# Optimization experiments

Measured on AMD Instinct MI355X. Metric: run time of the kernel, lower is better.

The kernel has to match this reference:

```python
import jax, jax.numpy as jnp
import numpy as np

B, S, D_MODEL = 2, 2048, 2048
N_HEADS, N_KV_HEADS = 32, 8
HEAD_DIM = D_MODEL // N_HEADS  # 64


def setup_inputs() -> dict:
    key = jax.random.key(0)
    ks = jax.random.split(key, 7)
    # rope frequencies (as in standard RoPE; values just need to be the right shape)
    inv_freq = 1.0 / (10000.0 ** (jnp.arange(0, HEAD_DIM, 2, dtype=jnp.float32) / HEAD_DIM))
    t = jnp.arange(S, dtype=jnp.float32)
    freqs = t[:, None] * inv_freq[None, :]  # (S, head_dim//2)
    scale = 0.02
    return {
        "x": jax.random.normal(ks[0], (B, S, D_MODEL), jnp.float32),
        "cos": jnp.cos(freqs),
        "sin": jnp.sin(freqs),
        "Wq": jax.random.normal(ks[1], (N_HEADS * HEAD_DIM, D_MODEL), jnp.float32) * scale,
        "Wk": jax.random.normal(ks[2], (N_KV_HEADS * HEAD_DIM, D_MODEL), jnp.float32) * scale,
        "Wv": jax.random.normal(ks[3], (N_KV_HEADS * HEAD_DIM, D_MODEL), jnp.float32) * scale,
        "Wo": jax.random.normal(ks[4], (D_MODEL, D_MODEL), jnp.float32) * scale,
    }


def _apply_rope(x, cos, sin):
    # x: (B, H, S, D); cos/sin: (S, D//2)
    d = x.shape[-1]
    x1, x2 = x[..., : d // 2], x[..., d // 2:]
    c = cos[None, None]
    s = sin[None, None]
    return jnp.concatenate([x1 * c - x2 * s, x1 * s + x2 * c], axis=-1)


def reference(x, cos, sin, Wq, Wk, Wv, Wo):
    b, s, _ = x.shape
    hd = 2 * cos.shape[-1]
    h = Wq.shape[0] // hd
    kv = Wk.shape[0] // hd
    g = h // kv  # query heads per kv head

    q = (x @ Wq.T).reshape(b, s, h, hd).transpose(0, 2, 1, 3)    # (b,h,s,d)
    k = (x @ Wk.T).reshape(b, s, kv, hd).transpose(0, 2, 1, 3)   # (b,kv,s,d)
    v = (x @ Wv.T).reshape(b, s, kv, hd).transpose(0, 2, 1, 3)

    q = _apply_rope(q, cos, sin)
    k = _apply_rope(k, cos, sin)

    # GQA: group query heads instead of materializing repeated K/V
    qg = q.reshape(b, kv, g, s, hd)
    scale = 1.0 / jnp.sqrt(jnp.asarray(hd, x.dtype))
    scores = jnp.einsum('bkgsd,bktd->bkgst', qg, k) * scale      # (b,kv,g,s,s)
    causal = jnp.arange(s)[:, None] >= jnp.arange(s)[None, :]
    scores = jnp.where(causal[None, None, None], scores, jnp.asarray(-jnp.inf, scores.dtype))
    attn = jax.nn.softmax(scores, axis=-1)
    out = jnp.einsum('bkgst,bktd->bkgsd', attn, v)               # (b,kv,g,s,d)
    out = out.reshape(b, h, s, hd).transpose(0, 2, 1, 3).reshape(b, s, h * hd)
    return out @ Wo.T
```

## Files before the change

kernel.cpp:

```cpp
#include <hip/hip_runtime.h>
#include <hip/hip_bf16.h>

typedef __bf16 bf16;
typedef __attribute__((ext_vector_type(8))) __bf16 bf16x8;
typedef __attribute__((ext_vector_type(4))) __bf16 bf16x4;
typedef __attribute__((ext_vector_type(4))) float f32x4;

#define B_SZ 2
#define S_SZ 2048
#define D_SZ 2048
#define H_SZ 32
#define KV_SZ 8
#define HD_SZ 64
#define M_SZ (B_SZ * S_SZ)
#define NQKV 3072

#define GLDS(g, s) __builtin_amdgcn_global_load_lds( \
    (const __attribute__((address_space(1))) void*)(g), \
    (__attribute__((address_space(3))) void*)(s), 16, 0, 0)

__device__ __forceinline__ void bar_lgkm() {
    asm volatile("s_waitcnt lgkmcnt(0)\n\ts_barrier" ::: "memory");
}

__global__ void cvt_all(const float* __restrict__ x, const float* __restrict__ Wq,
                        const float* __restrict__ Wk, const float* __restrict__ Wv,
                        const float* __restrict__ Wo,
                        bf16* __restrict__ xb, bf16* __restrict__ Wf, bf16* __restrict__ wob,
                        int nx, int n1, int n2) {
    int i = blockIdx.x * blockDim.x + threadIdx.x;
    const float* src; bf16* dst; int off;
    if (i < nx)                 { src = x;  dst = xb; off = i; }
    else {
        int j = i - nx;
        if (j < n1)             { src = Wq; dst = Wf; off = j; }
        else if (j < n1 + n2)   { src = Wk; dst = Wf + (size_t)4 * n1; off = j - n1; }
        else if (j < n1 + 2*n2) { src = Wv; dst = Wf + (size_t)4 * (n1 + n2); off = j - n1 - n2; }
        else if (j < 2*n1+2*n2) { src = Wo; dst = wob; off = j - n1 - 2 * n2; }
        else return;
    }
    float4 v = ((const float4*)src)[off];
    bf16x4 o;
    o.x = (bf16)v.x; o.y = (bf16)v.y; o.z = (bf16)v.z; o.w = (bf16)v.w;
    ((bf16x4*)dst)[off] = o;
}

#define GEMM_CORE2(A_, B_, Kdim)                                                 \
    const int tid  = threadIdx.x;                                                \
    const int w    = tid >> 6;                                                   \
    const int lane = tid & 63;                                                   \
    const int c = lane & 15, quad = lane >> 4;                                   \
    const int g8 = lane >> 3;                                                    \
    const int chs = ((lane & 7) ^ g8) * 8;                                       \
    const int rowBase = blockIdx.y * 128;                                        \
    const int colBase = blockIdx.x * 128;                                        \
    const bf16* Ag = A_ + (size_t)(rowBase + w * 64 + g8) * Kdim + chs;          \
    const bf16* Bg = B_ + (size_t)(colBase + w * 64 + g8) * Kdim + chs;          \
    bf16* sAw = As + (w * 64) * 64;                                              \
    bf16* sBw = Bs + (w * 64) * 64;                                              \
    f32x4 acc[4][8] = {};                                                        \
    for (int k0 = 0; k0 < Kdim; k0 += 64) {                                      \
        _Pragma("unroll")                                                        \
        for (int j = 0; j < 8; j++) {                                            \
            GLDS(Ag + (size_t)(j * 8) * Kdim + k0, sAw + j * 512);               \
            GLDS(Bg + (size_t)(j * 8) * Kdim + k0, sBw + j * 512);               \
        }                                                                        \
        __syncthreads();                                                         \
        _Pragma("unroll")                                                        \
        for (int ks = 0; ks < 2; ks++) {                                         \
            bf16x8 af[4], bfr[8];                                                \
            _Pragma("unroll")                                                    \
            for (int mi = 0; mi < 4; mi++)                                       \
                af[mi] = *(const bf16x8*)(As + (w * 64 + mi * 16 + c) * 64       \
                                          + (((ks << 2) + quad) ^ (c & 7)) * 8); \
            _Pragma("unroll")                                                    \
            for (int ni = 0; ni < 8; ni++)                                       \
                bfr[ni] = *(const bf16x8*)(Bs + (ni * 16 + c) * 64               \
                                          + (((ks << 2) + quad) ^ (c & 7)) * 8); \
            _Pragma("unroll")                                                    \
            for (int mi = 0; mi < 4; mi++)                                       \
                _Pragma("unroll")                                                \
                for (int ni = 0; ni < 8; ni++)                                   \
                    acc[mi][ni] = __builtin_amdgcn_mfma_f32_16x16x32_bf16(       \
                        af[mi], bfr[ni], acc[mi][ni], 0, 0, 0);                  \
        }                                                                        \
        __syncthreads();                                                         \
    }                                                                            \
    const int mBase = rowBase + w * 64;

__global__ __launch_bounds__(128, 2)
void gemm_qkv(const bf16* __restrict__ A, const bf16* __restrict__ Bw,
              bf16* __restrict__ Qb, bf16* __restrict__ Kb, bf16* __restrict__ Vtb,
              const float* __restrict__ cosp, const float* __restrict__ sinp,
              float qscale)
{
    __shared__ __align__(16) bf16 As[128 * 64];
    __shared__ __align__(16) bf16 Bs[128 * 64];

    GEMM_CORE2(A, Bw, D_SZ)

#pragma unroll
    for (int half = 0; half < 2; half++) {
        const int hcol = colBase + half * 64;
        const int no   = half * 4;
        if (hcol < 2560) {
            bf16* dst; int hh, Hn; float sc;
            if (hcol < 2048) { dst = Qb; hh = hcol >> 6;        Hn = H_SZ;  sc = qscale; }
            else             { dst = Kb; hh = (hcol >> 6) - 32; Hn = KV_SZ; sc = 1.0f;  }
#pragma unroll
            for (int mi = 0; mi < 4; mi++) {
#pragma unroll
                for (int r = 0; r < 4; r++) {
                    int row = mBase + mi * 16 + quad * 4 + r;
                    int b = row >> 11;
                    int s = row & 2047;
                    const float* cr = cosp + (size_t)s * 32;
                    const float* sr = sinp + (size_t)s * 32;
                    size_t base = ((size_t)(b * Hn + hh) * S_SZ + s) * 64;
#pragma unroll
                    for (int nj = 0; nj < 2; nj++) {
                        int d = nj * 16 + c;
                        float x1 = acc[mi][no + nj][r];
                        float x2 = acc[mi][no + nj + 2][r];
                        float cv = cr[d], sv = sr[d];
                        dst[base + d]      = (bf16)((x1 * cv - x2 * sv) * sc);
                        dst[base + d + 32] = (bf16)((x1 * sv + x2 * cv) * sc);
                    }
                }
            }
        } else {
            const int kvh = (hcol >> 6) - 40;
            const int b   = mBase >> 11;
            const int s0  = mBase & 2047;
#pragma unroll
            for (int nj = 0; nj < 4; nj++) {
                int d = nj * 16 + c;
                size_t base = ((size_t)(b * KV_SZ + kvh) * 64 + d) * (size_t)S_SZ;
#pragma unroll
                for (int mi = 0; mi < 4; mi++) {
                    int s = s0 + mi * 16 + quad * 4;
#pragma unroll
                    for (int r = 0; r < 4; r++)
                        Vtb[base + s + r] = (bf16)acc[mi][no + nj][r];
                }
            }
        }
    }
}

__global__ __launch_bounds__(128, 2)
void gemm_out(const bf16* __restrict__ A, const bf16* __restrict__ Bw,
              float* __restrict__ Co, int N, int K)
{
    __shared__ __align__(16) bf16 As[128 * 64];
    __shared__ __align__(16) bf16 Bs[128 * 64];

    GEMM_CORE2(A, Bw, K)

#pragma unroll
    for (int mi = 0; mi < 4; mi++)
#pragma unroll
        for (int ni = 0; ni < 8; ni++) {
            int col = colBase + ni * 16 + c;
#pragma unroll
            for (int r = 0; r < 4; r++) {
                int row = mBase + mi * 16 + quad * 4 + r;
                Co[(size_t)row * N + col] = acc[mi][ni][r];
            }
        }
}

#define PST 72

__global__ __launch_bounds__(256, 3)
void flash_attn(const bf16* __restrict__ Q, const bf16* __restrict__ Kc,
                const bf16* __restrict__ Vt, bf16* __restrict__ Aout)
{
    __shared__ __align__(16) bf16 Ks[64 * 64];
    __shared__ __align__(16) bf16 Vs[64 * 64];
    __shared__ __align__(16) bf16 Ps[2 * 4 * 16 * PST];

    const int tid  = threadIdx.x;
    const int lane = tid & 63;
    const int wave = tid >> 6;
    const int c = lane & 15, quad = lane >> 4;
    const int qloc = wave * 16 + c;

    const int i  = (blockIdx.x + blockIdx.y) & 15;
    const int tA = 31 - i, tB = i;
    const int q0A = tA << 6, q0B = tB << 6;

    const int bh = blockIdx.y;
    const int b  = bh >> 5;
    const int h  = bh & 31;
    const int kv = h >> 2;

    const bf16* Qp = Q  + (size_t)bh * (S_SZ * 64);
    const bf16* Kp = Kc + (size_t)(b * KV_SZ + kv) * (S_SZ * 64);
    const bf16* Vp = Vt + (size_t)(b * KV_SZ + kv) * (64 * S_SZ);

    bf16x8 aqA[2], aqB[2];
    {
        const bf16* qa = Qp + (size_t)(q0A + qloc) * 64 + quad * 8;
        aqA[0] = *(const bf16x8*)qa;  aqA[1] = *(const bf16x8*)(qa + 32);
        const bf16* qb = Qp + (size_t)(q0B + qloc) * 64 + quad * 8;
        aqB[0] = *(const bf16x8*)qb;  aqB[1] = *(const bf16x8*)(qb + 32);
    }

    f32x4 oA[4] = {}, oB[4] = {};
    f32x4 lA = {}, lB = {};

    bf16x8 ones;
#pragma unroll
    for (int j = 0; j < 8; j++) ones[j] = (bf16)1.0f;

    const int srow = tid >> 3;
    const int ch   = tid & 7;
    const int sws  = (ch ^ (srow & 7)) * 8;
    const bf16* Kg0 = Kp + (size_t)srow * 64 + ch * 8;
    const bf16* Kg1 = Kp + (size_t)(srow + 32) * 64 + ch * 8;
    const bf16* Vg0 = Vp + (size_t)srow * S_SZ + ch * 8;
    const bf16* Vg1 = Vp + (size_t)(srow + 32) * S_SZ + ch * 8;

    uint4 pk0 = *(const uint4*)Kg0, pk1 = *(const uint4*)Kg1;
    uint4 pv0 = *(const uint4*)Vg0, pv1 = *(const uint4*)Vg1;

    bf16* PwA = Ps + wave * 16 * PST;
    bf16* PwB = Ps + (4 + wave) * 16 * PST;

    for (int kt = 0; kt <= tA; kt++) {
        *(uint4*)(Ks + srow * 64 + sws)        = pk0;
        *(uint4*)(Ks + (srow + 32) * 64 + sws) = pk1;
        *(uint4*)(Vs + srow * 64 + sws)        = pv0;
        *(uint4*)(Vs + (srow + 32) * 64 + sws) = pv1;
        if (kt < tA) {
            pk0 = *(const uint4*)(Kg0 + (size_t)(kt + 1) * 4096);
            pk1 = *(const uint4*)(Kg1 + (size_t)(kt + 1) * 4096);
            pv0 = *(const uint4*)(Vg0 + (kt + 1) * 64);
            pv1 = *(const uint4*)(Vg1 + (kt + 1) * 64);
        }
        bar_lgkm();

        const bool doB   = (kt <= tB);
        const bool diagA = (kt == tA);
        const bool diagB = (kt == tB);

        f32x4 scA[4] = {}, scB[4] = {};
#pragma unroll
        for (int ks = 0; ks < 2; ks++) {
            bf16x8 ak4[4];
#pragma unroll
            for (int ni = 0; ni < 4; ni++)
                ak4[ni] = *(const bf16x8*)(Ks + (ni * 16 + c) * 64
                                           + (((ks << 2) + quad) ^ (c & 7)) * 8);
            __builtin_amdgcn_s_setprio(1);
#pragma unroll
            for (int ni = 0; ni < 4; ni++)
                scA[ni] = __builtin_amdgcn_mfma_f32_16x16x32_bf16(ak4[ni], aqA[ks], scA[ni], 0, 0, 0);
            if (doB) {
#pragma unroll
                for (int ni = 0; ni < 4; ni++)
                    scB[ni] = __builtin_amdgcn_mfma_f32_16x16x32_bf16(ak4[ni], aqB[ks], scB[ni], 0, 0, 0);
            }
            __builtin_amdgcn_s_setprio(0);
        }

        if (diagA) {
#pragma unroll
            for (int ni = 0; ni < 4; ni++) {
                bf16x4 pk;
#pragma unroll
                for (int r = 0; r < 4; r++) {
                    float p = exp2f(scA[ni][r]);
                    if ((ni * 16 + quad * 4 + r) > qloc) p = 0.f;
                    pk[r] = (bf16)p;
                }
                *(bf16x4*)(PwA + c * PST + ni * 16 + quad * 4) = pk;
            }
        } else {
#pragma unroll
            for (int ni = 0; ni < 4; ni++) {
                bf16x4 pk;
#pragma unroll
                for (int r = 0; r < 4; r++) pk[r] = (bf16)exp2f(scA[ni][r]);
                *(bf16x4*)(PwA + c * PST + ni * 16 + quad * 4) = pk;
            }
        }
        if (doB) {
            if (diagB) {
#pragma unroll
                for (int ni = 0; ni < 4; ni++) {
                    bf16x4 pk;
#pragma unroll
                    for (int r = 0; r < 4; r++) {
                        float p = exp2f(scB[ni][r]);
                        if ((ni * 16 + quad * 4 + r) > qloc) p = 0.f;
                        pk[r] = (bf16)p;
                    }
                    *(bf16x4*)(PwB + c * PST + ni * 16 + quad * 4) = pk;
                }
            } else {
#pragma unroll
                for (int ni = 0; ni < 4; ni++) {
                    bf16x4 pk;
#pragma unroll
                    for (int r = 0; r < 4; r++) pk[r] = (bf16)exp2f(scB[ni][r]);
                    *(bf16x4*)(PwB + c * PST + ni * 16 + quad * 4) = pk;
                }
            }
        }

#pragma unroll
        for (int ks = 0; ks < 2; ks++) {
            bf16x8 av4[4];
#pragma unroll
            for (int ni = 0; ni < 4; ni++)
                av4[ni] = *(const bf16x8*)(Vs + (ni * 16 + c) * 64
                                           + (((ks << 2) + quad) ^ (c & 7)) * 8);
            bf16x8 bpA = *(const bf16x8*)(PwA + c * PST + ks * 32 + quad * 8);
            __builtin_amdgcn_s_setprio(1);
            lA = __builtin_amdgcn_mfma_f32_16x16x32_bf16(ones, bpA, lA, 0, 0, 0);
#pragma unroll
            for (int ni = 0; ni < 4; ni++)
                oA[ni] = __builtin_amdgcn_mfma_f32_16x16x32_bf16(av4[ni], bpA, oA[ni], 0, 0, 0);
            __builtin_amdgcn_s_setprio(0);
            if (doB) {
                bf16x8 bpB = *(const bf16x8*)(PwB + c * PST + ks * 32 + quad * 8);
                __builtin_amdgcn_s_setprio(1);
                lB = __builtin_amdgcn_mfma_f32_16x16x32_bf16(ones, bpB, lB, 0, 0, 0);
#pragma unroll
                for (int ni = 0; ni < 4; ni++)
                    oB[ni] = __builtin_amdgcn_mfma_f32_16x16x32_bf16(av4[ni], bpB, oB[ni], 0, 0, 0);
                __builtin_amdgcn_s_setprio(0);
            }
        }
        bar_lgkm();
    }

    {
        float ila = 1.f / lA[0];
        float ilb = 1.f / lB[0];
        bf16* pa = Aout + ((size_t)(b * S_SZ + q0A + qloc)) * D_SZ + h * 64;
        bf16* pb = Aout + ((size_t)(b * S_SZ + q0B + qloc)) * D_SZ + h * 64;
#pragma unroll
        for (int ni = 0; ni < 4; ni++) {
            bf16x4 wa, wb;
#pragma unroll
            for (int r = 0; r < 4; r++) {
                wa[r] = (bf16)(oA[ni][r] * ila);
                wb[r] = (bf16)(oB[ni][r] * ilb);
            }
            *(bf16x4*)(pa + ni * 16 + quad * 4) = wa;
            *(bf16x4*)(pb + ni * 16 + quad * 4) = wb;
        }
    }
}

extern "C" void kernel_launch(void* const* d_in, const int* in_sizes, int n_in,
                              void* d_out, int out_size, void* d_ws, size_t ws_size,
                              hipStream_t stream) {
    const float* x    = (const float*)d_in[0];
    const float* cosp = (const float*)d_in[1];
    const float* sinp = (const float*)d_in[2];
    const float* Wq   = (const float*)d_in[3];
    const float* Wk   = (const float*)d_in[4];
    const float* Wv   = (const float*)d_in[5];
    const float* Wo   = (const float*)d_in[6];
    float* out = (float*)d_out;

    const int M = M_SZ;
    const int D = D_SZ;
    const int NKV = KV_SZ * HD_SZ;

    bf16* xb   = (bf16*)d_ws;
    bf16* Wf   = xb  + (size_t)M * D;
    bf16* Qb   = Wf  + (size_t)NQKV * D;
    bf16* Kb   = Qb  + (size_t)M * D;
    bf16* Vtb  = Kb  + (size_t)B_SZ * KV_SZ * S_SZ * 64;
    bf16* wob  = Vtb + (size_t)B_SZ * KV_SZ * 64 * S_SZ;
    bf16* attn = xb;

    const int nx = M * D / 4, n1 = D * D / 4, n2 = NKV * D / 4;

    cvt_all<<<(nx + 2 * n1 + 2 * n2 + 255) / 256, 256, 0, stream>>>(
        x, Wq, Wk, Wv, Wo, xb, Wf, wob, nx, n1, n2);

    const float qscale = 0.125f * 1.44269504089f;

    gemm_qkv<<<dim3(NQKV / 128, M / 128), 128, 0, stream>>>(xb, Wf, Qb, Kb, Vtb, cosp, sinp, qscale);

    flash_attn<<<dim3(16, B_SZ * H_SZ), 256, 0, stream>>>(Qb, Kb, Vtb, attn);

    gemm_out<<<dim3(D / 128, M / 128), 128, 0, stream>>>(attn, wob, out, D, D);
}
```

Before: 297.2 us.

## Split GEMM 128x128 tiles across four waves in a 2x2 layout

```diff
diff --git a/kernel.cpp b/kernel.cpp
--- a/kernel.cpp
+++ b/kernel.cpp
@@ -45,50 +45,52 @@
     ((bf16x4*)dst)[off] = o;
 }
 
-#define GEMM_CORE2(A_, B_, Kdim)                                                 \
+#define GEMM_CORE4(A_, B_, Kdim)                                                 \
     const int tid  = threadIdx.x;                                                \
-    const int w    = tid >> 6;                                                   \
+    const int wv   = tid >> 6;                                                   \
     const int lane = tid & 63;                                                   \
     const int c = lane & 15, quad = lane >> 4;                                   \
+    const int wr = wv >> 1, wc = wv & 1;                                         \
     const int g8 = lane >> 3;                                                    \
     const int chs = ((lane & 7) ^ g8) * 8;                                       \
     const int rowBase = blockIdx.y * 128;                                        \
     const int colBase = blockIdx.x * 128;                                        \
-    const bf16* Ag = A_ + (size_t)(rowBase + w * 64 + g8) * Kdim + chs;          \
-    const bf16* Bg = B_ + (size_t)(colBase + w * 64 + g8) * Kdim + chs;          \
-    bf16* sAw = As + (w * 64) * 64;                                              \
-    bf16* sBw = Bs + (w * 64) * 64;                                              \
-    f32x4 acc[4][8] = {};                                                        \
+    const bf16* Ag = A_ + (size_t)(rowBase + wv * 32 + g8) * Kdim + chs;         \
+    const bf16* Bg = B_ + (size_t)(colBase + wv * 32 + g8) * Kdim + chs;         \
+    bf16* sAw = As + (wv * 32) * 64;                                             \
+    bf16* sBw = Bs + (wv * 32) * 64;                                             \
+    f32x4 acc[4][4] = {};                                                        \
     for (int k0 = 0; k0 < Kdim; k0 += 64) {                                      \
         _Pragma("unroll")                                                        \
-        for (int j = 0; j < 8; j++) {                                            \
+        for (int j = 0; j < 4; j++) {                                            \
             GLDS(Ag + (size_t)(j * 8) * Kdim + k0, sAw + j * 512);               \
             GLDS(Bg + (size_t)(j * 8) * Kdim + k0, sBw + j * 512);               \
         }                                                                        \
         __syncthreads();                                                         \
         _Pragma("unroll")                                                        \
         for (int ks = 0; ks < 2; ks++) {                                         \
-            bf16x8 af[4], bfr[8];                                                \
+            bf16x8 af[4], bfr[4];                                                \
             _Pragma("unroll")                                                    \
             for (int mi = 0; mi < 4; mi++)                                       \
-                af[mi] = *(const bf16x8*)(As + (w * 64 + mi * 16 + c) * 64       \
+                af[mi] = *(const bf16x8*)(As + (wr * 64 + mi * 16 + c) * 64      \
                                           + (((ks << 2) + quad) ^ (c & 7)) * 8); \
             _Pragma("unroll")                                                    \
-            for (int ni = 0; ni < 8; ni++)                                       \
-                bfr[ni] = *(const bf16x8*)(Bs + (ni * 16 + c) * 64               \
+            for (int ni = 0; ni < 4; ni++)                                       \
+                bfr[ni] = *(const bf16x8*)(Bs + (wc * 64 + ni * 16 + c) * 64     \
                                           + (((ks << 2) + quad) ^ (c & 7)) * 8); \
             _Pragma("unroll")                                                    \
             for (int mi = 0; mi < 4; mi++)                                       \
                 _Pragma("unroll")                                                \
-                for (int ni = 0; ni < 8; ni++)                                   \
+                for (int ni = 0; ni < 4; ni++)                                   \
                     acc[mi][ni] = __builtin_amdgcn_mfma_f32_16x16x32_bf16(       \
                         af[mi], bfr[ni], acc[mi][ni], 0, 0, 0);                  \
         }                                                                        \
         __syncthreads();                                                         \
     }                                                                            \
-    const int mBase = rowBase + w * 64;
-
-__global__ __launch_bounds__(128, 2)
+    const int mBase = rowBase + wr * 64;                                         \
+    const int nBase = colBase + wc * 64;
+
+__global__ __launch_bounds__(256, 2)
 void gemm_qkv(const bf16* __restrict__ A, const bf16* __restrict__ Bw,
               bf16* __restrict__ Qb, bf16* __restrict__ Kb, bf16* __restrict__ Vtb,
               const float* __restrict__ cosp, const float* __restrict__ sinp,
@@ -97,71 +99,67 @@
     __shared__ __align__(16) bf16 As[128 * 64];
     __shared__ __align__(16) bf16 Bs[128 * 64];
 
-    GEMM_CORE2(A, Bw, D_SZ)
-
-#pragma unroll
-    for (int half = 0; half < 2; half++) {
-        const int hcol = colBase + half * 64;
-        const int no   = half * 4;
-        if (hcol < 2560) {
-            bf16* dst; int hh, Hn; float sc;
-            if (hcol < 2048) { dst = Qb; hh = hcol >> 6;        Hn = H_SZ;  sc = qscale; }
-            else             { dst = Kb; hh = (hcol >> 6) - 32; Hn = KV_SZ; sc = 1.0f;  }
+    GEMM_CORE4(A, Bw, D_SZ)
+
+    const int hcol = nBase;
+    if (hcol < 2560) {
+        bf16* dst; int hh, Hn; float sc;
+        if (hcol < 2048) { dst = Qb; hh = hcol >> 6;        Hn = H_SZ;  sc = qscale; }
+        else             { dst = Kb; hh = (hcol >> 6) - 32; Hn = KV_SZ; sc = 1.0f;  }
+#pragma unroll
+        for (int mi = 0; mi < 4; mi++) {
+#pragma unroll
+            for (int r = 0; r < 4; r++) {
+                int row = mBase + mi * 16 + quad * 4 + r;
+                int b = row >> 11;
+                int s = row & 2047;
+                const float* cr = cosp + (size_t)s * 32;
+                const float* sr = sinp + (size_t)s * 32;
+                size_t base = ((size_t)(b * Hn + hh) * S_SZ + s) * 64;
+#pragma unroll
+                for (int nj = 0; nj < 2; nj++) {
+                    int d = nj * 16 + c;
+                    float x1 = acc[mi][nj][r];
+                    float x2 = acc[mi][nj + 2][r];
+                    float cv = cr[d], sv = sr[d];
+                    dst[base + d]      = (bf16)((x1 * cv - x2 * sv) * sc);
+                    dst[base + d + 32] = (bf16)((x1 * sv + x2 * cv) * sc);
+                }
+            }
+        }
+    } else {
+        const int kvh = (hcol >> 6) - 40;
+        const int b   = mBase >> 11;
+        const int s0  = mBase & 2047;
+#pragma unroll
+        for (int nj = 0; nj < 4; nj++) {
+            int d = nj * 16 + c;
+            size_t base = ((size_t)(b * KV_SZ + kvh) * 64 + d) * (size_t)S_SZ;
 #pragma unroll
             for (int mi = 0; mi < 4; mi++) {
-#pragma unroll
-                for (int r = 0; r < 4; r++) {
-                    int row = mBase + mi * 16 + quad * 4 + r;
-                    int b = row >> 11;
-                    int s = row & 2047;
-                    const float* cr = cosp + (size_t)s * 32;
-                    const float* sr = sinp + (size_t)s * 32;
-                    size_t base = ((size_t)(b * Hn + hh) * S_SZ + s) * 64;
-#pragma unroll
-                    for (int nj = 0; nj < 2; nj++) {
-                        int d = nj * 16 + c;
-                        float x1 = acc[mi][no + nj][r];
-                        float x2 = acc[mi][no + nj + 2][r];
-                        float cv = cr[d], sv = sr[d];
-                        dst[base + d]      = (bf16)((x1 * cv - x2 * sv) * sc);
-                        dst[base + d + 32] = (bf16)((x1 * sv + x2 * cv) * sc);
-                    }
-                }
-            }
-        } else {
-            const int kvh = (hcol >> 6) - 40;
-            const int b   = mBase >> 11;
-            const int s0  = mBase & 2047;
-#pragma unroll
-            for (int nj = 0; nj < 4; nj++) {
-                int d = nj * 16 + c;
-                size_t base = ((size_t)(b * KV_SZ + kvh) * 64 + d) * (size_t)S_SZ;
-#pragma unroll
-                for (int mi = 0; mi < 4; mi++) {
-                    int s = s0 + mi * 16 + quad * 4;
-#pragma unroll
-                    for (int r = 0; r < 4; r++)
-                        Vtb[base + s + r] = (bf16)acc[mi][no + nj][r];
-                }
-            }
-        }
-    }
-}
-
-__global__ __launch_bounds__(128, 2)
+                int s = s0 + mi * 16 + quad * 4;
+#pragma unroll
+                for (int r = 0; r < 4; r++)
+                    Vtb[base + s + r] = (bf16)acc[mi][nj][r];
+            }
+        }
+    }
+}
+
+__global__ __launch_bounds__(256, 2)
 void gemm_out(const bf16* __restrict__ A, const bf16* __restrict__ Bw,
               float* __restrict__ Co, int N, int K)
 {
     __shared__ __align__(16) bf16 As[128 * 64];
     __shared__ __align__(16) bf16 Bs[128 * 64];
 
-    GEMM_CORE2(A, Bw, K)
+    GEMM_CORE4(A, Bw, K)
 
 #pragma unroll
     for (int mi = 0; mi < 4; mi++)
 #pragma unroll
-        for (int ni = 0; ni < 8; ni++) {
-            int col = colBase + ni * 16 + c;
+        for (int ni = 0; ni < 4; ni++) {
+            int col = nBase + ni * 16 + c;
 #pragma unroll
             for (int r = 0; r < 4; r++) {
                 int row = mBase + mi * 16 + quad * 4 + r;
@@ -387,9 +385,9 @@
 
     const float qscale = 0.125f * 1.44269504089f;
 
-    gemm_qkv<<<dim3(NQKV / 128, M / 128), 128, 0, stream>>>(xb, Wf, Qb, Kb, Vtb, cosp, sinp, qscale);
+    gemm_qkv<<<dim3(NQKV / 128, M / 128), 256, 0, stream>>>(xb, Wf, Qb, Kb, Vtb, cosp, sinp, qscale);
 
     flash_attn<<<dim3(16, B_SZ * H_SZ), 256, 0, stream>>>(Qb, Kb, Vtb, attn);
 
-    gemm_out<<<dim3(D / 128, M / 128), 128, 0, stream>>>(attn, wob, out, D, D);
-}
+    gemm_out<<<dim3(D / 128, M / 128), 256, 0, stream>>>(attn, wob, out, D, D);
+}
```

After: 294.7 us. About the same (-0.8%).
